# Kernel optimization log

Measured on AMD Instinct MI355X. Metric: run time of the kernel, lower is better.

## Reference

```python
import jax, jax.numpy as jnp
import numpy as np

# BoxCoder weights and clamp from the torch module
WX, WY, WW, WH = 10.0, 10.0, 5.0, 5.0
BBOX_CLIP = float(np.log(1000.0 / 16.0))
SCORE_THRESH = 0.05
NMS_THRESH = 0.5
DET_PER_IMG = 100
MIN_SIZE = 0.01
B, N, C = 4, 4096, 91
IMG_H, IMG_W = 800, 1216


def setup_inputs() -> dict:
    key = jax.random.key(0)
    k1, k2, k3, k4, k5, k6 = jax.random.split(key, 6)
    class_logits = jax.random.normal(k1, (B * N, C), dtype=jnp.float32) * 2.0
    box_regression = jax.random.normal(k2, (B * N, C * 4), dtype=jnp.float32) * 0.5
    # valid xyxy proposals inside the image
    x1 = jax.random.uniform(k3, (B, N)) * (0.7 * IMG_W)
    y1 = jax.random.uniform(k4, (B, N)) * (0.7 * IMG_H)
    bw = jax.random.uniform(k5, (B, N)) * (0.25 * IMG_W) + 4.0
    bh = jax.random.uniform(k6, (B, N)) * (0.25 * IMG_H) + 4.0
    proposals = jnp.stack([x1, y1, x1 + bw, y1 + bh], axis=-1)
    image_shapes = jnp.tile(jnp.array([[IMG_H, IMG_W]], dtype=jnp.int32), (B, 1))
    return {"class_logits": class_logits, "box_regression": box_regression,
            "proposals": proposals, "image_shapes": image_shapes}


def decode_boxes(deltas, proposals):
    # deltas [N, C, 4], proposals [N, 4] xyxy -> pred boxes [N, C, 4]
    w = proposals[:, 2] - proposals[:, 0]
    h = proposals[:, 3] - proposals[:, 1]
    cx = proposals[:, 0] + 0.5 * w
    cy = proposals[:, 1] + 0.5 * h
    dx = deltas[..., 0] / WX
    dy = deltas[..., 1] / WY
    dw = jnp.minimum(deltas[..., 2] / WW, BBOX_CLIP)
    dh = jnp.minimum(deltas[..., 3] / WH, BBOX_CLIP)
    pcx = dx * w[:, None] + cx[:, None]
    pcy = dy * h[:, None] + cy[:, None]
    pw = jnp.exp(dw) * w[:, None]
    ph = jnp.exp(dh) * h[:, None]
    return jnp.stack([pcx - 0.5 * pw, pcy - 0.5 * ph,
                      pcx + 0.5 * pw, pcy + 0.5 * ph], axis=-1)


def iou_one_many(box, boxes):
    # box [4] vs boxes [M, 4]
    lt = jnp.maximum(box[:2], boxes[:, :2])
    rb = jnp.minimum(box[2:], boxes[:, 2:])
    wh = jnp.clip(rb - lt, 0.0)
    inter = wh[:, 0] * wh[:, 1]
    a1 = (box[2] - box[0]) * (box[3] - box[1])
    a2 = (boxes[:, 2] - boxes[:, 0]) * (boxes[:, 3] - boxes[:, 1])
    return inter / (a1 + a2 - inter)


def nms_keep(off_boxes, live):
    # greedy NMS on class-offset boxes; selection is non-differentiable
    off_boxes = jax.lax.stop_gradient(off_boxes)
    live = jax.lax.stop_gradient(live)

    def body(lv, _):
        i = jnp.argmax(lv)
        s = lv[i]
        iou = iou_one_many(off_boxes[i], off_boxes)
        lv = jnp.where(iou > NMS_THRESH, -jnp.inf, lv)
        lv = lv.at[i].set(-jnp.inf)
        return lv, (i, jnp.isfinite(s))

    _, (keep, kvalid) = jax.lax.scan(body, live, None, length=DET_PER_IMG)
    return keep, kvalid  # [DET_PER_IMG] each


def postprocess_one(logits, deltas, proposals, hw):
    # logits [N, C], deltas [N, C*4], proposals [N, 4], hw [2] float (H, W)
    num_classes = logits.shape[-1]
    boxes = decode_boxes(deltas.reshape(-1, num_classes, 4), proposals)  # [N, C, 4]
    Hh, Ww = hw[0], hw[1]
    boxes = jnp.stack([jnp.clip(boxes[..., 0], 0.0, Ww),
                       jnp.clip(boxes[..., 1], 0.0, Hh),
                       jnp.clip(boxes[..., 2], 0.0, Ww),
                       jnp.clip(boxes[..., 3], 0.0, Hh)], axis=-1)
    scores = jax.nn.softmax(logits, axis=-1)
    labels = jnp.broadcast_to(jnp.arange(num_classes, dtype=jnp.int32), scores.shape)
    # drop background class 0, flatten per-class candidates -> M = N*(C-1)
    boxes = boxes[:, 1:].reshape(-1, 4)
    scores = scores[:, 1:].reshape(-1)
    labels = labels[:, 1:].reshape(-1)
    ws = boxes[:, 2] - boxes[:, 0]
    hs = boxes[:, 3] - boxes[:, 1]
    valid = (scores > SCORE_THRESH) & (ws >= MIN_SIZE) & (hs >= MIN_SIZE)
    # batched_nms: per-class coordinate offset so classes never overlap
    max_coord = jnp.max(boxes)
    off_boxes = boxes + (labels.astype(boxes.dtype) * (max_coord + 1.0))[:, None]
    live = jnp.where(valid, scores, -jnp.inf)
    keep, kvalid = nms_keep(off_boxes, live)
    out_boxes = jnp.where(kvalid[:, None], boxes[keep], 0.0)
    out_scores = jnp.where(kvalid, scores[keep], 0.0)
    out_labels = jnp.where(kvalid, labels[keep], -1)
    return out_boxes, out_scores, out_labels


def reference(class_logits, box_regression, proposals, image_shapes):
    b, n, _ = proposals.shape
    num_classes = class_logits.shape[-1]
    logits = class_logits.reshape(b, n, num_classes)
    deltas = box_regression.reshape(b, n, num_classes * 4)
    hw = image_shapes.astype(logits.dtype)
    boxes, scores, labels = jax.vmap(postprocess_one)(logits, deltas, proposals, hw)
    return boxes, scores, labels
```

## Files before the change

### kernel.cpp

```cpp
#include <hip/hip_runtime.h>
#include <math.h>
#include <float.h>
#include <limits.h>

#define NBATCH 4
#define NPROP  4096
#define NCLS   91
#define NFG    90
#define NDET   100
#define CCAP   1024
#define BN     (NBATCH * NPROP)
#define SLOTS  (NFG * NDET)
#define FCAP   16384

static __device__ __forceinline__ float clampf(float x, float lo, float hi) {
    return fminf(fmaxf(x, lo), hi);
}

static __device__ __forceinline__ void decode_box(int b, int np, int c,
    const float* __restrict__ props, const float* __restrict__ deltas,
    float W, float H, float& bx1, float& by1, float& bx2, float& by2)
{
    const float* pr = props + ((size_t)b * NPROP + np) * 4;
    const float x1 = pr[0], y1 = pr[1], x2 = pr[2], y2 = pr[3];
    const float w = x2 - x1, h = y2 - y1;
    const float cx = x1 + 0.5f * w, cy = y1 + 0.5f * h;
    const float* d = deltas + (((size_t)b * NPROP + np) * NCLS + c) * 4;
    const float BBC = 4.135166556742356f;
    const float dx = d[0] / 10.0f;
    const float dy = d[1] / 10.0f;
    const float dw = fminf(d[2] / 5.0f, BBC);
    const float dh = fminf(d[3] / 5.0f, BBC);
    const float pcx = dx * w + cx;
    const float pcy = dy * h + cy;
    const float pw = expf(dw) * w;
    const float ph = expf(dh) * h;
    bx1 = clampf(pcx - 0.5f * pw, 0.0f, W);
    by1 = clampf(pcy - 0.5f * ph, 0.0f, H);
    bx2 = clampf(pcx + 0.5f * pw, 0.0f, W);
    by2 = clampf(pcy + 0.5f * ph, 0.0f, H);
}

static __device__ __forceinline__ int block_excl_scan(int v, int t, int* wtot)
{
    const int lane = t & 63, wid = t >> 6;
    int inc = v;
    #pragma unroll
    for (int s = 1; s < 64; s <<= 1) {
        const int u = __shfl_up(inc, s);
        if (lane >= s) inc += u;
    }
    if (lane == 63) wtot[wid] = inc;
    __syncthreads();
    int base = 0;
    for (int w2 = 0; w2 < wid; ++w2) base += wtot[w2];
    __syncthreads();
    return base + inc - v;
}

__global__ __launch_bounds__(256) void stats_mask_kernel(
    const float* __restrict__ logits, const float* __restrict__ props,
    const float* __restrict__ deltas, const int* __restrict__ imgsh,
    float2* __restrict__ stats, unsigned* __restrict__ mask)
{
    const int wavei = threadIdx.x >> 6;
    const int lane  = threadIdx.x & 63;
    const int p = blockIdx.x * 4 + wavei;
    const int b = p >> 12;
    const int np = p & (NPROP - 1);
    const float* lrow = logits + (size_t)p * NCLS;

    const float a  = lrow[lane];
    const float a2 = (lane + 64 < NCLS) ? lrow[lane + 64] : -INFINITY;

    float m = fmaxf(a, a2);
    #pragma unroll
    for (int s = 32; s > 0; s >>= 1) m = fmaxf(m, __shfl_down(m, s));
    m = __shfl(m, 0);

    const float e0 = expf(a - m);
    const float e1 = (lane + 64 < NCLS) ? expf(a2 - m) : 0.0f;
    float sum = e0 + e1;
    #pragma unroll
    for (int s = 32; s > 0; s >>= 1) sum += __shfl_down(sum, s);
    sum = __shfl(sum, 0);

    const float W = (float)imgsh[b * 2 + 1];
    const float H = (float)imgsh[b * 2 + 0];

    bool pass0 = ((e0 / sum) > 0.05f) && (lane >= 1);
    if (pass0) {
        float bx1, by1, bx2, by2;
        decode_box(b, np, lane, props, deltas, W, H, bx1, by1, bx2, by2);
        pass0 = ((bx2 - bx1) >= 0.01f) && ((by2 - by1) >= 0.01f);
    }
    bool pass1 = ((e1 / sum) > 0.05f);
    if (pass1) {
        float bx1, by1, bx2, by2;
        decode_box(b, np, lane + 64, props, deltas, W, H, bx1, by1, bx2, by2);
        pass1 = ((bx2 - bx1) >= 0.01f) && ((by2 - by1) >= 0.01f);
    }

    const unsigned long long b0 = __ballot(pass0);
    const unsigned long long b1 = __ballot(pass1);

    if (lane == 0) {
        stats[p] = make_float2(m, sum);
        mask[p]          = (unsigned)b0;
        mask[BN + p]     = (unsigned)(b0 >> 32);
        mask[2 * BN + p] = (unsigned)b1;
    }
}

__global__ __launch_bounds__(256) void class_nms_kernel(
    const float* __restrict__ logits, const float2* __restrict__ stats,
    const unsigned* __restrict__ mask,
    const float* __restrict__ props, const float* __restrict__ deltas,
    const int* __restrict__ imgsh, unsigned long long* __restrict__ svKeys)
{
    const int blk  = blockIdx.x;
    const int b    = blk / NFG;
    const int cm1  = blk % NFG;
    const int c    = cm1 + 1;
    const int t    = threadIdx.x;
    const int lane = t & 63;
    const int wid  = t >> 6;

    __shared__ unsigned long long sk[CCAP];
    __shared__ float4 sbox[CCAP];
    __shared__ int wtot[4];

    const float W = (float)imgsh[b * 2 + 1];
    const float H = (float)imgsh[b * 2 + 0];

    const unsigned* mp = mask + (size_t)(c >> 5) * BN + b * NPROP;
    const unsigned bit = 1u << (c & 31);

    int cnt = 0;
    #pragma unroll 4
    for (int np = t; np < NPROP; np += 256) cnt += (mp[np] & bit) ? 1 : 0;

    int v = cnt;
    #pragma unroll
    for (int s = 1; s < 64; s <<= 1) {
        const int u = __shfl_up(v, s);
        if (lane >= s) v += u;
    }
    if (lane == 63) wtot[wid] = v;
    __syncthreads();
    int base = 0;
    for (int w2 = 0; w2 < wid; ++w2) base += wtot[w2];
    int pos = base + v - cnt;
    const int ntot = wtot[0] + wtot[1] + wtot[2] + wtot[3];
    const int n = min(ntot, CCAP);
    if (n == 0) {
        for (int i = t; i < NDET; i += 256) svKeys[(size_t)blk * NDET + i] = 0ULL;
        return;
    }

    for (int np = t; np < NPROP; np += 256) {
        if (!(mp[np] & bit)) continue;
        const int p = b * NPROP + np;
        const float lg = logits[(size_t)p * NCLS + c];
        const float2 st = stats[p];
        const float score = expf(lg - st.x) / st.y;
        const unsigned flat = (unsigned)(np * NFG + cm1);
        const unsigned long long key =
            ((unsigned long long)__float_as_uint(score) << 32) | (unsigned)(~flat);
        if (pos < CCAP) sk[pos] = key;
        ++pos;
    }
    __syncthreads();

    int P = 1; while (P < n) P <<= 1;
    for (int i = n + t; i < P; i += 256) sk[i] = 0ULL;

    for (unsigned kk = 2; kk <= (unsigned)P; kk <<= 1) {
        for (unsigned jj = kk >> 1; jj > 0; jj >>= 1) {
            __syncthreads();
            for (unsigned i = t; i < (unsigned)P; i += 256) {
                const unsigned ixj = i ^ jj;
                if (ixj > i) {
                    const unsigned long long x = sk[i], y = sk[ixj];
                    const bool up = ((i & kk) == 0);
                    if (up ? (x < y) : (x > y)) { sk[i] = y; sk[ixj] = x; }
                }
            }
        }
    }
    __syncthreads();

    for (int i = t; i < n; i += 256) {
        const unsigned flat = ~(unsigned)sk[i];
        const int np = flat / NFG;
        float bx1, by1, bx2, by2;
        decode_box(b, np, c, props, deltas, W, H, bx1, by1, bx2, by2);
        sbox[i] = make_float4(bx1, by1, bx2, by2);
    }
    __syncthreads();

    if (t >= 64) return;
    float4 own0 = make_float4(0.f, 0.f, 0.f, 0.f);
    float4 own1 = make_float4(0.f, 0.f, 0.f, 0.f);
    int ns = 0;
    unsigned long long kcur = sk[0];
    float4 bcur = sbox[0];
    for (int i = 0; i < n && ns < NDET; ++i) {
        const unsigned long long key = kcur;
        const float4 Q = bcur;
        const int j = i + 1;
        if (j < n) { kcur = sk[j]; bcur = sbox[j]; }
        const float aq = (Q.z - Q.x) * (Q.w - Q.y);
        const float iw0 = fmaxf(fminf(own0.z, Q.z) - fmaxf(own0.x, Q.x), 0.0f);
        const float ih0 = fmaxf(fminf(own0.w, Q.w) - fmaxf(own0.y, Q.y), 0.0f);
        const float in0 = iw0 * ih0;
        const float as0 = (own0.z - own0.x) * (own0.w - own0.y);
        const float iw1 = fmaxf(fminf(own1.z, Q.z) - fmaxf(own1.x, Q.x), 0.0f);
        const float ih1 = fmaxf(fminf(own1.w, Q.w) - fmaxf(own1.y, Q.y), 0.0f);
        const float in1 = iw1 * ih1;
        const float as1 = (own1.z - own1.x) * (own1.w - own1.y);
        const bool sup = (in0 / (as0 + aq - in0) > 0.5f) ||
                         (in1 / (as1 + aq - in1) > 0.5f);
        if (!__any(sup)) {
            if (lane == (ns & 63)) { if (ns < 64) own0 = Q; else own1 = Q; }
            if (lane == 0) svKeys[(size_t)blk * NDET + ns] = key;
            ++ns;
        }
    }
    for (int i = ns + lane; i < NDET; i += 64) svKeys[(size_t)blk * NDET + i] = 0ULL;
}

__global__ __launch_bounds__(1024) void select_kernel(
    const unsigned long long* __restrict__ svKeys,
    const float* __restrict__ props, const float* __restrict__ deltas,
    const int* __restrict__ imgsh, float* __restrict__ out)
{
    const int b = blockIdx.x;
    const int t = threadIdx.x;
    __shared__ unsigned long long F[FCAP];
    __shared__ int hist[4096];
    __shared__ int wtot[16];
    __shared__ int s_T, s_above, s_total;

    if (t == 0) { s_T = -1; s_above = 0; s_total = 0; }
    #pragma unroll
    for (int j = 0; j < 4; ++j) hist[t + j * 1024] = 0;

    const unsigned long long* src = svKeys + (size_t)b * SLOTS;
    unsigned long long keys[9];
    #pragma unroll
    for (int j = 0; j < 9; ++j) {
        const int s = t + j * 1024;
        keys[j] = (s < SLOTS) ? src[s] : 0ULL;
    }
    __syncthreads();

    #pragma unroll
    for (int j = 0; j < 9; ++j) {
        if (keys[j] != 0ULL) atomicAdd(&hist[(unsigned)(keys[j] >> 52)], 1);
    }
    __syncthreads();

    {
        const int gbase = (1023 - t) * 4;
        const int s0 = hist[gbase] + hist[gbase + 1] + hist[gbase + 2] + hist[gbase + 3];
        const int pre = block_excl_scan(s0, t, wtot);
        int acc = pre;
        for (int d = gbase + 3; d >= gbase; --d) {
            const int h = hist[d];
            if (acc < NDET && acc + h >= NDET) { s_T = d; s_above = acc; }
            acc += h;
        }
        if (t == 1023) s_total = acc;
    }
    __syncthreads();

    const int T = s_T;
    const int total = s_total;
    const int n2 = (T < 0) ? total : (s_above + hist[T]);
    const bool fast = (n2 <= 2048);

    int mycnt = 0;
    #pragma unroll
    for (int j = 0; j < 9; ++j) {
        const unsigned long long k = keys[j];
        const bool m = (k != 0ULL) && (fast ? (T < 0 || (int)(k >> 52) >= T) : true);
        mycnt += m ? 1 : 0;
    }
    int off = block_excl_scan(mycnt, t, wtot);
    #pragma unroll
    for (int j = 0; j < 9; ++j) {
        const unsigned long long k = keys[j];
        const bool m = (k != 0ULL) && (fast ? (T < 0 || (int)(k >> 52) >= T) : true);
        if (m) F[off++] = k;
    }
    const int nsort = fast ? n2 : total;

    int P = 128; while (P < nsort) P <<= 1;
    for (int i = nsort + t; i < P; i += 1024) F[i] = 0ULL;

    for (unsigned kk = 2; kk <= (unsigned)P; kk <<= 1) {
        for (unsigned jj = kk >> 1; jj > 0; jj >>= 1) {
            __syncthreads();
            for (unsigned i = t; i < (unsigned)P; i += 1024) {
                const unsigned ixj = i ^ jj;
                if (ixj > i) {
                    const unsigned long long x = F[i], y = F[ixj];
                    const bool up = ((i & kk) == 0);
                    if (up ? (x < y) : (x > y)) { F[i] = y; F[ixj] = x; }
                }
            }
        }
    }
    __syncthreads();

    float* oB = out + (size_t)b * NDET * 4;
    float* oS = out + (size_t)NBATCH * NDET * 4 + (size_t)b * NDET;
    float* oL = out + (size_t)NBATCH * NDET * 5 + (size_t)b * NDET;
    if (t < NDET) {
        const unsigned long long key = F[t];
        if (key != 0ULL) {
            const unsigned flat = ~(unsigned)key;
            const float score = __uint_as_float((unsigned)(key >> 32));
            const int np = flat / NFG;
            const int c  = (int)(flat - (unsigned)np * NFG) + 1;
            const float W = (float)imgsh[b * 2 + 1];
            const float H = (float)imgsh[b * 2 + 0];
            float bx1, by1, bx2, by2;
            decode_box(b, np, c, props, deltas, W, H, bx1, by1, bx2, by2);
            oB[t * 4 + 0] = bx1; oB[t * 4 + 1] = by1;
            oB[t * 4 + 2] = bx2; oB[t * 4 + 3] = by2;
            oS[t] = score;
            oL[t] = (float)c;
        } else {
            oB[t * 4 + 0] = 0.0f; oB[t * 4 + 1] = 0.0f;
            oB[t * 4 + 2] = 0.0f; oB[t * 4 + 3] = 0.0f;
            oS[t] = 0.0f; oL[t] = -1.0f;
        }
    }
}

extern "C" void kernel_launch(void* const* d_in, const int* in_sizes, int n_in,
                              void* d_out, int out_size, void* d_ws, size_t ws_size,
                              hipStream_t stream)
{
    const float* logits = (const float*)d_in[0];
    const float* deltas = (const float*)d_in[1];
    const float* props  = (const float*)d_in[2];
    const int*   imgsh  = (const int*)d_in[3];
    float* out = (float*)d_out;

    char* w = (char*)d_ws;
    float2* stats = (float2*)w;            w += (size_t)BN * sizeof(float2);
    unsigned* mask = (unsigned*)w;         w += (size_t)3 * BN * sizeof(unsigned);
    unsigned long long* svKeys = (unsigned long long*)w;
    w += (size_t)NBATCH * SLOTS * sizeof(unsigned long long);

    stats_mask_kernel<<<BN / 4, 256, 0, stream>>>(logits, props, deltas, imgsh, stats, mask);
    class_nms_kernel<<<NBATCH * NFG, 256, 0, stream>>>(
        logits, stats, mask, props, deltas, imgsh, svKeys);
    select_kernel<<<NBATCH, 1024, 0, stream>>>(svKeys, props, deltas, imgsh, out);
}
```

Measured before the change: 87.08 us.

## Split per-class NMS into separate sort and single-wave sweep kernels

Splits the per-class kernel in two. The first kernel (256 threads) compacts and bitonic-sorts the candidate keys, then writes them and the count to global workspace. A second kernel with 64-thread blocks reloads the keys, decodes boxes and runs the serial greedy sweep, so three idle waves are no longer held during the long single-wave phase and LDS use per block drops. The cost is an extra launch, a global round trip for the sorted keys, and box decode done by only 64 threads.

```diff
diff --git a/kernel.cpp b/kernel.cpp
--- a/kernel.cpp
+++ b/kernel.cpp
@@ -112,11 +112,10 @@
     }
 }
 
-__global__ __launch_bounds__(256) void class_nms_kernel(
+__global__ __launch_bounds__(256) void class_sort_kernel(
     const float* __restrict__ logits, const float2* __restrict__ stats,
     const unsigned* __restrict__ mask,
-    const float* __restrict__ props, const float* __restrict__ deltas,
-    const int* __restrict__ imgsh, unsigned long long* __restrict__ svKeys)
+    int* __restrict__ gN, unsigned long long* __restrict__ gKeys)
 {
     const int blk  = blockIdx.x;
     const int b    = blk / NFG;
@@ -127,11 +126,7 @@
     const int wid  = t >> 6;
 
     __shared__ unsigned long long sk[CCAP];
-    __shared__ float4 sbox[CCAP];
     __shared__ int wtot[4];
-
-    const float W = (float)imgsh[b * 2 + 1];
-    const float H = (float)imgsh[b * 2 + 0];
 
     const unsigned* mp = mask + (size_t)(c >> 5) * BN + b * NPROP;
     const unsigned bit = 1u << (c & 31);
@@ -153,10 +148,8 @@
     int pos = base + v - cnt;
     const int ntot = wtot[0] + wtot[1] + wtot[2] + wtot[3];
     const int n = min(ntot, CCAP);
-    if (n == 0) {
-        for (int i = t; i < NDET; i += 256) svKeys[(size_t)blk * NDET + i] = 0ULL;
-        return;
-    }
+    if (t == 0) gN[blk] = n;
+    if (n == 0) return;
 
     for (int np = t; np < NPROP; np += 256) {
         if (!(mp[np] & bit)) continue;
@@ -190,8 +183,36 @@
     }
     __syncthreads();
 
-    for (int i = t; i < n; i += 256) {
-        const unsigned flat = ~(unsigned)sk[i];
+    for (int i = t; i < n; i += 256) gKeys[(size_t)blk * CCAP + i] = sk[i];
+}
+
+__global__ __launch_bounds__(64) void class_sweep_kernel(
+    const int* __restrict__ gN, const unsigned long long* __restrict__ gKeys,
+    const float* __restrict__ props, const float* __restrict__ deltas,
+    const int* __restrict__ imgsh, unsigned long long* __restrict__ svKeys)
+{
+    const int blk  = blockIdx.x;
+    const int b    = blk / NFG;
+    const int cm1  = blk % NFG;
+    const int c    = cm1 + 1;
+    const int lane = threadIdx.x;
+
+    __shared__ unsigned long long sk[CCAP];
+    __shared__ float4 sbox[CCAP];
+
+    const int n = gN[blk];
+    if (n == 0) {
+        for (int i = lane; i < NDET; i += 64) svKeys[(size_t)blk * NDET + i] = 0ULL;
+        return;
+    }
+
+    const float W = (float)imgsh[b * 2 + 1];
+    const float H = (float)imgsh[b * 2 + 0];
+
+    for (int i = lane; i < n; i += 64) {
+        const unsigned long long key = gKeys[(size_t)blk * CCAP + i];
+        sk[i] = key;
+        const unsigned flat = ~(unsigned)key;
         const int np = flat / NFG;
         float bx1, by1, bx2, by2;
         decode_box(b, np, c, props, deltas, W, H, bx1, by1, bx2, by2);
@@ -199,7 +220,6 @@
     }
     __syncthreads();
 
-    if (t >= 64) return;
     float4 own0 = make_float4(0.f, 0.f, 0.f, 0.f);
     float4 own1 = make_float4(0.f, 0.f, 0.f, 0.f);
     int ns = 0;
@@ -355,9 +375,12 @@
     unsigned* mask = (unsigned*)w;         w += (size_t)3 * BN * sizeof(unsigned);
     unsigned long long* svKeys = (unsigned long long*)w;
     w += (size_t)NBATCH * SLOTS * sizeof(unsigned long long);
+    int* gN = (int*)w;                     w += 4096;
+    unsigned long long* gKeys = (unsigned long long*)w;
+    w += (size_t)NBATCH * NFG * CCAP * sizeof(unsigned long long);
 
     stats_mask_kernel<<<BN / 4, 256, 0, stream>>>(logits, props, deltas, imgsh, stats, mask);
-    class_nms_kernel<<<NBATCH * NFG, 256, 0, stream>>>(
-        logits, stats, mask, props, deltas, imgsh, svKeys);
+    class_sort_kernel<<<NBATCH * NFG, 256, 0, stream>>>(logits, stats, mask, gN, gKeys);
+    class_sweep_kernel<<<NBATCH * NFG, 64, 0, stream>>>(gN, gKeys, props, deltas, imgsh, svKeys);
     select_kernel<<<NBATCH, 1024, 0, stream>>>(svKeys, props, deltas, imgsh, out);
 }
```

Result: slower. 90.41 us (+3.8%).

## Replace serial per-class NMS loop with chunked bitmask NMS across the block

Applied to the files above, without the earlier changes.

Replaces the single-wavefront greedy NMS scan, which tests each candidate against all kept boxes one by one, with a chunked scheme. For each chunk of 128 sorted candidates, all 256 threads test the candidates against the already kept boxes and build a pairwise suppression bitmask within the chunk. Thread 0 then resolves the chunk serially using bit operations. This spreads the IoU work across the whole block, at the cost of extra block-wide barriers per chunk, a serial single-thread resolve step, and IoU work on candidates the old loop never reached because it stopped early.

```diff
diff --git a/kernel.cpp b/kernel.cpp
--- a/kernel.cpp
+++ b/kernel.cpp
@@ -12,6 +12,7 @@
 #define BN     (NBATCH * NPROP)
 #define SLOTS  (NFG * NDET)
 #define FCAP   16384
+#define CHUNK  128
 
 static __device__ __forceinline__ float clampf(float x, float lo, float hi) {
     return fminf(fmaxf(x, lo), hi);
@@ -41,6 +42,15 @@
     by2 = clampf(pcy + 0.5f * ph, 0.0f, H);
 }
 
+static __device__ __forceinline__ bool iou_gt(const float4 S, const float4 Q, float aq)
+{
+    const float iw = fmaxf(fminf(S.z, Q.z) - fmaxf(S.x, Q.x), 0.0f);
+    const float ih = fmaxf(fminf(S.w, Q.w) - fmaxf(S.y, Q.y), 0.0f);
+    const float inter = iw * ih;
+    const float as = (S.z - S.x) * (S.w - S.y);
+    return inter / (as + aq - inter) > 0.5f;
+}
+
 static __device__ __forceinline__ int block_excl_scan(int v, int t, int* wtot)
 {
     const int lane = t & 63, wid = t >> 6;
@@ -128,7 +138,11 @@
 
     __shared__ unsigned long long sk[CCAP];
     __shared__ float4 sbox[CCAP];
+    __shared__ unsigned long long mrow[CHUNK][2];
+    __shared__ float4 sOwn[NDET];
+    __shared__ unsigned long long sPreW[2];
     __shared__ int wtot[4];
+    __shared__ int s_ns;
 
     const float W = (float)imgsh[b * 2 + 1];
     const float H = (float)imgsh[b * 2 + 0];
@@ -197,37 +211,66 @@
         decode_box(b, np, c, props, deltas, W, H, bx1, by1, bx2, by2);
         sbox[i] = make_float4(bx1, by1, bx2, by2);
     }
-    __syncthreads();
-
-    if (t >= 64) return;
-    float4 own0 = make_float4(0.f, 0.f, 0.f, 0.f);
-    float4 own1 = make_float4(0.f, 0.f, 0.f, 0.f);
-    int ns = 0;
-    unsigned long long kcur = sk[0];
-    float4 bcur = sbox[0];
-    for (int i = 0; i < n && ns < NDET; ++i) {
-        const unsigned long long key = kcur;
-        const float4 Q = bcur;
-        const int j = i + 1;
-        if (j < n) { kcur = sk[j]; bcur = sbox[j]; }
-        const float aq = (Q.z - Q.x) * (Q.w - Q.y);
-        const float iw0 = fmaxf(fminf(own0.z, Q.z) - fmaxf(own0.x, Q.x), 0.0f);
-        const float ih0 = fmaxf(fminf(own0.w, Q.w) - fmaxf(own0.y, Q.y), 0.0f);
-        const float in0 = iw0 * ih0;
-        const float as0 = (own0.z - own0.x) * (own0.w - own0.y);
-        const float iw1 = fmaxf(fminf(own1.z, Q.z) - fmaxf(own1.x, Q.x), 0.0f);
-        const float ih1 = fmaxf(fminf(own1.w, Q.w) - fmaxf(own1.y, Q.y), 0.0f);
-        const float in1 = iw1 * ih1;
-        const float as1 = (own1.z - own1.x) * (own1.w - own1.y);
-        const bool sup = (in0 / (as0 + aq - in0) > 0.5f) ||
-                         (in1 / (as1 + aq - in1) > 0.5f);
-        if (!__any(sup)) {
-            if (lane == (ns & 63)) { if (ns < 64) own0 = Q; else own1 = Q; }
-            if (lane == 0) svKeys[(size_t)blk * NDET + ns] = key;
-            ++ns;
-        }
-    }
-    for (int i = ns + lane; i < NDET; i += 64) svKeys[(size_t)blk * NDET + i] = 0ULL;
+    if (t == 0) s_ns = 0;
+    __syncthreads();
+
+    int nsTot = 0;
+    for (int cb = 0; cb < n && nsTot < NDET; cb += CHUNK) {
+        const int C = min(CHUNK, n - cb);
+
+        bool pre = false;
+        if (t < C) {
+            const float4 Q = sbox[cb + t];
+            const float aq = (Q.z - Q.x) * (Q.w - Q.y);
+            for (int l = 0; l < nsTot; ++l) {
+                if (iou_gt(sOwn[l], Q, aq)) { pre = true; break; }
+            }
+        }
+        const unsigned long long bal = __ballot(pre);
+        if (t == 0)  sPreW[0] = bal;
+        if (t == 64) sPreW[1] = bal;
+
+        {
+            const int r = t >> 1, w = t & 1;
+            unsigned long long word = 0ULL;
+            if (r < C) {
+                const float4 R = sbox[cb + r];
+                const int j0 = w * 64;
+                const int jend = min(j0 + 64, C);
+                for (int j = (j0 > r + 1 ? j0 : r + 1); j < jend; ++j) {
+                    const float4 Q = sbox[cb + j];
+                    const float aq = (Q.z - Q.x) * (Q.w - Q.y);
+                    if (iou_gt(R, Q, aq)) word |= (1ULL << (j - j0));
+                }
+            }
+            mrow[r][w] = word;
+        }
+        __syncthreads();
+
+        if (t == 0) {
+            unsigned long long S0 = sPreW[0], S1 = sPreW[1];
+            int ns = nsTot;
+            unsigned long long r0 = mrow[0][0], r1 = mrow[0][1];
+            for (int i = 0; i < C && ns < NDET; ++i) {
+                const unsigned long long nr0 = (i + 1 < C) ? mrow[i + 1][0] : 0ULL;
+                const unsigned long long nr1 = (i + 1 < C) ? mrow[i + 1][1] : 0ULL;
+                const bool dead = (i < 64) ? ((S0 >> i) & 1ULL)
+                                           : ((S1 >> (i - 64)) & 1ULL);
+                if (!dead) {
+                    sOwn[ns] = sbox[cb + i];
+                    svKeys[(size_t)blk * NDET + ns] = sk[cb + i];
+                    ++ns;
+                    S0 |= r0; S1 |= r1;
+                }
+                r0 = nr0; r1 = nr1;
+            }
+            s_ns = ns;
+        }
+        __syncthreads();
+        nsTot = s_ns;
+    }
+
+    for (int i = nsTot + t; i < NDET; i += 256) svKeys[(size_t)blk * NDET + i] = 0ULL;
 }
 
 __global__ __launch_bounds__(1024) void select_kernel(
```

After: 80.09 us. 1.09x faster.
